# Optimization experiments

Hardware: AMD Instinct MI355X
Metric: run time of the kernel (lower is better)

The kernel has to match this reference:

```python
import jax, jax.numpy as jnp
import numpy as np

B, N, ND, ED, HD = 2, 384, 128, 32, 128
MSG_IN = 2 * ND + ED + 1  # 289
LN_EPS = 1e-3  # keras LayerNormalization default epsilon


def setup_inputs() -> dict:
    key = jax.random.key(0)
    ks = jax.random.split(key, 20)
    s = 0.05
    return {
        "h": jax.random.normal(ks[0], (B, N, ND), jnp.float32),
        "x": jax.random.normal(ks[1], (B, N, 3), jnp.float32),
        "edge_attr": jax.random.normal(ks[2], (B, N, N, ED), jnp.float32),
        "atom_mask": jnp.ones((B, N), jnp.float32),
        "msg_w1": jax.random.normal(ks[3], (MSG_IN, HD), jnp.float32) * s,
        "msg_b1": jnp.zeros((HD,), jnp.float32),
        "msg_w2": jax.random.normal(ks[4], (HD, HD), jnp.float32) * s,
        "msg_b2": jnp.zeros((HD,), jnp.float32),
        "node_w1": jax.random.normal(ks[5], (ND + HD, HD), jnp.float32) * s,
        "node_b1": jnp.zeros((HD,), jnp.float32),
        "node_w2": jax.random.normal(ks[6], (HD, ND), jnp.float32) * s,
        "node_b2": jnp.zeros((ND,), jnp.float32),
        "coord_w1": jax.random.normal(ks[7], (HD, HD), jnp.float32) * s,
        "coord_b1": jnp.zeros((HD,), jnp.float32),
        "coord_w2": jax.random.normal(ks[8], (HD, 1), jnp.float32) * 0.01,  # RandomNormal(0, 0.01)
        "ln_gamma": jnp.ones((ND,), jnp.float32),
        "ln_beta": jnp.zeros((ND,), jnp.float32),
        "adj": jax.random.randint(ks[9], (B, N, N), 0, 2, jnp.int32),
    }


def _layernorm(y, gamma, beta):
    mu = jnp.mean(y, axis=-1, keepdims=True)
    var = jnp.mean(jnp.square(y - mu), axis=-1, keepdims=True)
    return (y - mu) * jax.lax.rsqrt(var + LN_EPS) * gamma + beta


def reference(h, x, edge_attr, atom_mask,
              msg_w1, msg_b1, msg_w2, msg_b2,
              node_w1, node_b1, node_w2, node_b2,
              coord_w1, coord_b1, coord_w2,
              ln_gamma, ln_beta, adj):
    n = h.shape[1]
    rel_pos = x[:, :, None, :] - x[:, None, :, :]              # [B,N,N,3]
    dist_sq = jnp.sum(rel_pos ** 2, axis=-1, keepdims=True)    # [B,N,N,1]
    h_i = jnp.broadcast_to(h[:, :, None, :], (h.shape[0], n, n, h.shape[-1]))
    h_j = jnp.broadcast_to(h[:, None, :, :], (h.shape[0], n, n, h.shape[-1]))
    msg_in = jnp.concatenate([h_i, h_j, edge_attr, dist_sq], axis=-1)  # [B,N,N,289]
    m = jax.nn.silu(msg_in @ msg_w1 + msg_b1)
    m = jax.nn.silu(m @ msg_w2 + msg_b2)                        # [B,N,N,HD]
    adj_f = adj.astype(m.dtype)[..., None]                      # [B,N,N,1]
    m = m * adj_f
    h_agg = jnp.sum(m, axis=2)                                  # [B,N,HD]
    u = jax.nn.silu(jnp.concatenate([h, h_agg], axis=-1) @ node_w1 + node_b1)
    h_update = u @ node_w2 + node_b2
    h_new = _layernorm(h + h_update, ln_gamma, ln_beta)
    # coordinate update
    cw = jax.nn.silu(m @ coord_w1 + coord_b1) @ coord_w2        # [B,N,N,1]
    dist = jnp.sqrt(dist_sq + 1e-8)
    cw = cw / (dist + 1.0) * adj_f
    x_agg = jnp.sum(cw * rel_pos, axis=2) * atom_mask[..., None]
    x_new = x + x_agg
    return (h_new, x_new)
```

## Files before the change

### kernel.cpp

```cpp
#include <hip/hip_runtime.h>

typedef float f32x4 __attribute__((ext_vector_type(4)));
typedef unsigned int u32x4 __attribute__((ext_vector_type(4)));
typedef unsigned int u32x2 __attribute__((ext_vector_type(2)));
typedef __bf16 bf16x8 __attribute__((ext_vector_type(8)));

#define LDS_WET   0
#define LDS_W2T   10240
#define LDS_WC1T  45056
#define LDS_ACTW  79872
#define LDS_FP    114688
#define LDS_CIDX  117760
#define LDS_WCNT  118528
#define LDS_BYTES 118596

__device__ __forceinline__ unsigned short f2bf(float f) {
  unsigned int u = __builtin_bit_cast(unsigned int, f);
  unsigned int r = u + 0x7FFFu + ((u >> 16) & 1u);
  return (unsigned short)(r >> 16);
}
__device__ __forceinline__ unsigned int pk2(float lo, float hi) {
  unsigned short a = __builtin_bit_cast(unsigned short, (__bf16)lo);
  unsigned short b = __builtin_bit_cast(unsigned short, (__bf16)hi);
  return (unsigned int)a | ((unsigned int)b << 16);
}
__device__ __forceinline__ short bf1(float f) {
  return (short)__builtin_bit_cast(unsigned short, (__bf16)f);
}
__device__ __forceinline__ float bflo(unsigned int u) {
  return __builtin_bit_cast(float, u << 16);
}
__device__ __forceinline__ float bfhi(unsigned int u) {
  return __builtin_bit_cast(float, u & 0xFFFF0000u);
}
__device__ __forceinline__ float silu_f(float xv) {
  float t = __builtin_amdgcn_exp2f(-1.44269504088896f * xv);
  return xv * __builtin_amdgcn_rcpf(1.0f + t);
}
__device__ __forceinline__ f32x4 mfma16(u32x4 a, u32x4 b, f32x4 c) {
  return __builtin_amdgcn_mfma_f32_16x16x32_bf16(
      __builtin_bit_cast(bf16x8, a), __builtin_bit_cast(bf16x8, b), c, 0, 0, 0);
}

__global__ void egnn_pre(const float* __restrict__ h,
                         const float* __restrict__ msg_w1,
                         const float* __restrict__ msg_b1,
                         float* __restrict__ his,
                         unsigned short* __restrict__ hjw) {
  __shared__ float hr[128];
  const int row = blockIdx.x;
  const int t = threadIdx.x;
  if (t < 128) hr[t] = h[(size_t)row*128 + t];
  __syncthreads();
  const int col = t & 127;
  const int base = (t < 128) ? 0 : 128;
  float s = (t < 128) ? msg_b1[col] : 0.0f;
  #pragma unroll 4
  for (int k = 0; k < 128; ++k) s += hr[k] * msg_w1[(size_t)(base + k)*128 + col];
  if (t < 128) his[(size_t)row*128 + col] = s;
  else         hjw[(size_t)row*128 + col] = f2bf(s);
}

__launch_bounds__(512, 1)
__global__ void egnn_main(
    const float* __restrict__ h, const float* __restrict__ x,
    const float* __restrict__ eattr, const float* __restrict__ amask,
    const float* __restrict__ msg_w1, const float* __restrict__ msg_w2,
    const float* __restrict__ msg_b2, const float* __restrict__ node_w1,
    const float* __restrict__ node_b1, const float* __restrict__ node_w2,
    const float* __restrict__ node_b2, const float* __restrict__ coord_w1,
    const float* __restrict__ coord_b1, const float* __restrict__ coord_w2,
    const float* __restrict__ ln_g, const float* __restrict__ ln_b,
    const int* __restrict__ adj, const float* __restrict__ his,
    const unsigned short* __restrict__ hjw, float* __restrict__ out)
{
  extern __shared__ char smem[];
  short* weT  = (short*)(smem + LDS_WET);
  short* w2T  = (short*)(smem + LDS_W2T);
  short* wc1T = (short*)(smem + LDS_WC1T);
  float* fp   = (float*)(smem + LDS_FP);
  float* HisL = fp;          float* wdL  = fp + 128;
  float* b2L  = fp + 256;    float* bc1L = fp + 384;
  float* wc2L = fp + 512;    float* hrow = fp + 640;
  unsigned short* cidx16 = (unsigned short*)(smem + LDS_CIDX);
  int* wcnt = (int*)(smem + LDS_WCNT);
  int* wsc  = wcnt + 8;

  const int tid  = threadIdx.x;
  const int bi   = blockIdx.x;
  const int bb   = (bi / 384) * 384;
  const int wave = tid >> 6;
  const int lane = tid & 63;
  const int g    = lane >> 4;
  const int lr   = lane & 15;
  short* actW = (short*)(smem + LDS_ACTW) + wave*(16*136);

  const bool pred = (tid < 384) && (adj[(size_t)bi*384 + tid] != 0);
  const unsigned long long bmask = __ballot(pred);
  if (lane == 0) wcnt[wave] = __popcll(bmask);

  for (int idx = tid; idx < 32*128; idx += 512) {
    int k = idx >> 7, d = idx & 127;
    weT[d*40 + k] = bf1(msg_w1[(size_t)(256 + k)*128 + d]);
  }
  for (int idx = tid; idx < 128*128; idx += 512) {
    int k = idx >> 7, d = idx & 127;
    w2T[d*136 + k]  = bf1(msg_w2[idx]);
    wc1T[d*136 + k] = bf1(coord_w1[idx]);
  }
  if (tid < 128) {
    HisL[tid] = his[(size_t)bi*128 + tid];
    wdL[tid]  = msg_w1[288*128 + tid];
    b2L[tid]  = msg_b2[tid];
    bc1L[tid] = coord_b1[tid];
    wc2L[tid] = coord_w2[tid];
    hrow[tid] = h[(size_t)bi*128 + tid];
  }
  __syncthreads();

  if (tid == 0) {
    int run = 0;
    #pragma unroll
    for (int w = 0; w < 8; ++w) { wsc[w] = run; run += wcnt[w]; }
    wsc[8] = run;
  }
  __syncthreads();
  if (pred) {
    int rank = __popcll(bmask & ((1ull << lane) - 1ull));
    cidx16[wsc[wave] + rank] = (unsigned short)tid;
  }
  const int deg = wsc[8];
  const float xi0 = x[bi*3+0], xi1 = x[bi*3+1], xi2 = x[bi*3+2];
  f32x4 hacc2[8];
  #pragma unroll
  for (int cf = 0; cf < 8; ++cf) hacc2[cf] = (f32x4){0.f, 0.f, 0.f, 0.f};
  float xc0 = 0.0f, xc1 = 0.0f, xc2 = 0.0f;
  __syncthreads();

  const int nchunk = (deg + 127) >> 7;
  for (int ch = 0; ch < nchunk; ++ch) {
    const int sbase = ch*128 + wave*16;
    if (sbase >= deg) continue;
    const int s = sbase + lr;
    const bool valid = (s < deg);
    const int cj = valid ? (int)cidx16[s] : 0;
    const float vm = valid ? 1.0f : 0.0f;
    const float* xp = x + (size_t)(bb + cj)*3;
    const float r0 = xi0 - xp[0], r1 = xi1 - xp[1], r2 = xi2 - xp[2];
    const float dq = r0*r0 + r1*r1 + r2*r2;
    const float fc = __builtin_amdgcn_rcpf(sqrtf(dq + 1e-8f) + 1.0f) * vm;
    const float c0 = fc*r0, c1 = fc*r1, c2 = fc*r2;
    const float* ep = eattr + ((size_t)bi*384 + cj)*32 + g*8;
    const float4 p0 = ((const float4*)ep)[0];
    const float4 p1 = ((const float4*)ep)[1];
    const u32x4 be = (u32x4){pk2(p0.x, p0.y), pk2(p0.z, p0.w),
                             pk2(p1.x, p1.y), pk2(p1.z, p1.w)};

    #pragma unroll
    for (int cf = 0; cf < 8; ++cf) {
      const int dO = cf*16 + 4*g;
      u32x2 hj = *(const u32x2*)(hjw + (size_t)(bb + cj)*128 + dO);
      f32x4 hv = *(const f32x4*)(HisL + dO);
      f32x4 wv = *(const f32x4*)(wdL + dO);
      f32x4 acc;
      acc[0] = hv[0] + dq*wv[0] + bflo(hj[0]);
      acc[1] = hv[1] + dq*wv[1] + bfhi(hj[0]);
      acc[2] = hv[2] + dq*wv[2] + bflo(hj[1]);
      acc[3] = hv[3] + dq*wv[3] + bfhi(hj[1]);
      u32x4 aw = *(const u32x4*)(weT + (cf*16 + lr)*40 + g*8);
      acc = mfma16(aw, be, acc);
      *(u32x2*)(actW + lr*136 + dO) =
          (u32x2){pk2(silu_f(acc[0]), silu_f(acc[1])),
                  pk2(silu_f(acc[2]), silu_f(acc[3]))};
    }

    u32x4 bk[4];
    #pragma unroll
    for (int kk = 0; kk < 4; ++kk)
      bk[kk] = *(const u32x4*)(actW + lr*136 + kk*32 + g*8);
    #pragma unroll
    for (int cf = 0; cf < 8; ++cf) {
      const int dO = cf*16 + 4*g;
      f32x4 a = *(const f32x4*)(b2L + dO);
      #pragma unroll
      for (int kk = 0; kk < 4; ++kk) {
        u32x4 aw2 = *(const u32x4*)(w2T + (cf*16 + lr)*136 + kk*32 + g*8);
        a = mfma16(aw2, bk[kk], a);
      }
      float v0 = silu_f(a[0]) * vm, v1 = silu_f(a[1]) * vm;
      float v2 = silu_f(a[2]) * vm, v3 = silu_f(a[3]) * vm;
      hacc2[cf][0] += v0; hacc2[cf][1] += v1;
      hacc2[cf][2] += v2; hacc2[cf][3] += v3;
      *(u32x2*)(actW + lr*136 + dO) = (u32x2){pk2(v0, v1), pk2(v2, v3)};
    }

    u32x4 bm[4];
    #pragma unroll
    for (int kk = 0; kk < 4; ++kk)
      bm[kk] = *(const u32x4*)(actW + lr*136 + kk*32 + g*8);
    float cwp = 0.0f;
    #pragma unroll
    for (int cf = 0; cf < 8; ++cf) {
      const int dO = cf*16 + 4*g;
      f32x4 a = *(const f32x4*)(bc1L + dO);
      #pragma unroll
      for (int kk = 0; kk < 4; ++kk) {
        u32x4 aw3 = *(const u32x4*)(wc1T + (cf*16 + lr)*136 + kk*32 + g*8);
        a = mfma16(aw3, bm[kk], a);
      }
      f32x4 wv = *(const f32x4*)(wc2L + dO);
      cwp += silu_f(a[0])*wv[0] + silu_f(a[1])*wv[1]
           + silu_f(a[2])*wv[2] + silu_f(a[3])*wv[3];
    }
    cwp += __shfl_xor(cwp, 16, 64);
    cwp += __shfl_xor(cwp, 32, 64);
    if (lane < 16) { xc0 += cwp*c0; xc1 += cwp*c1; xc2 += cwp*c2; }
  }

  __syncthreads();
  #pragma unroll
  for (int cf = 0; cf < 8; ++cf) {
    #pragma unroll
    for (int r = 0; r < 4; ++r) {
      float v = hacc2[cf][r];
      v += __shfl_xor(v, 1, 64); v += __shfl_xor(v, 2, 64);
      v += __shfl_xor(v, 4, 64); v += __shfl_xor(v, 8, 64);
      hacc2[cf][r] = v;
    }
  }
  float* actF  = (float*)(smem + LDS_ACTW);
  float* hpart = actF;
  float* xcf   = actF + 1024;
  float* red   = actF + 1408;
  float* hagg  = actF + 1920;
  float* uvec  = actF + 2048;
  float* lnr   = actF + 2176;
  if (lr == 0) {
    #pragma unroll
    for (int cf = 0; cf < 8; ++cf)
      #pragma unroll
      for (int r = 0; r < 4; ++r)
        hpart[wave*128 + cf*16 + 4*g + r] = hacc2[cf][r];
  }
  if (lane < 16) {
    const int idx = wave*16 + lr;
    xcf[idx] = xc0; xcf[128 + idx] = xc1; xcf[256 + idx] = xc2;
  }
  __syncthreads();
  if (tid < 128) {
    float s = 0.0f;
    #pragma unroll
    for (int w = 0; w < 8; ++w) s += hpart[w*128 + tid];
    hagg[tid] = s;
  }
  if (tid < 3) {
    float sx = 0.0f;
    #pragma unroll 8
    for (int j = 0; j < 128; ++j) sx += xcf[tid*128 + j];
    out[98304 + (size_t)bi*3 + tid] = x[bi*3 + tid] + sx * amask[bi];
  }
  __syncthreads();

  {
    const int d = tid & 127, q = tid >> 7;
    float s = 0.0f;
    for (int k = q*64; k < q*64 + 64; ++k) {
      const float inv = (k < 128) ? hrow[k] : hagg[k - 128];
      s += inv * node_w1[(size_t)k*128 + d];
    }
    red[q*128 + d] = s;
  }
  __syncthreads();
  if (tid < 128)
    uvec[tid] = silu_f(red[tid] + red[128+tid] + red[256+tid] + red[384+tid] + node_b1[tid]);
  __syncthreads();

  {
    const int d = tid & 127, q = tid >> 7;
    float s = 0.0f;
    for (int k = q*32; k < q*32 + 32; ++k) s += uvec[k] * node_w2[(size_t)k*128 + d];
    red[q*128 + d] = s;
  }
  __syncthreads();
  float y = 0.0f;
  if (tid < 128)
    y = hrow[tid] + red[tid] + red[128+tid] + red[256+tid] + red[384+tid] + node_b2[tid];

  float ssum = (tid < 128) ? y : 0.0f;
  #pragma unroll
  for (int mm = 1; mm < 64; mm <<= 1) ssum += __shfl_xor(ssum, mm, 64);
  if (tid < 128 && lane == 0) lnr[wave] = ssum;
  __syncthreads();
  const float mu = (lnr[0] + lnr[1]) * (1.0f/128.0f);
  float yc = (tid < 128) ? (y - mu) : 0.0f;
  float sq = yc * yc;
  #pragma unroll
  for (int mm = 1; mm < 64; mm <<= 1) sq += __shfl_xor(sq, mm, 64);
  if (tid < 128 && lane == 0) lnr[2 + wave] = sq;
  __syncthreads();
  if (tid < 128) {
    const float var = (lnr[2] + lnr[3]) * (1.0f/128.0f);
    out[(size_t)bi*128 + tid] = yc * rsqrtf(var + 1e-3f) * ln_g[tid] + ln_b[tid];
  }
}

extern "C" void kernel_launch(void* const* d_in, const int* in_sizes, int n_in,
                              void* d_out, int out_size, void* d_ws, size_t ws_size,
                              hipStream_t stream) {
  const float* h        = (const float*)d_in[0];
  const float* x        = (const float*)d_in[1];
  const float* eattr    = (const float*)d_in[2];
  const float* amask    = (const float*)d_in[3];
  const float* msg_w1   = (const float*)d_in[4];
  const float* msg_b1   = (const float*)d_in[5];
  const float* msg_w2   = (const float*)d_in[6];
  const float* msg_b2   = (const float*)d_in[7];
  const float* node_w1  = (const float*)d_in[8];
  const float* node_b1  = (const float*)d_in[9];
  const float* node_w2  = (const float*)d_in[10];
  const float* node_b2  = (const float*)d_in[11];
  const float* coord_w1 = (const float*)d_in[12];
  const float* coord_b1 = (const float*)d_in[13];
  const float* coord_w2 = (const float*)d_in[14];
  const float* ln_g     = (const float*)d_in[15];
  const float* ln_b     = (const float*)d_in[16];
  const int*   adj      = (const int*)d_in[17];
  float* out = (float*)d_out;
  float* his = (float*)d_ws;
  unsigned short* hjw = (unsigned short*)((char*)d_ws + 393216);

  hipFuncSetAttribute((const void*)egnn_main,
                      hipFuncAttributeMaxDynamicSharedMemorySize, LDS_BYTES);

  egnn_pre<<<768, 256, 0, stream>>>(h, msg_w1, msg_b1, his, hjw);
  egnn_main<<<768, 512, LDS_BYTES, stream>>>(h, x, eattr, amask, msg_w1, msg_w2,
      msg_b2, node_w1, node_b1, node_w2, node_b2, coord_w1, coord_b1, coord_w2,
      ln_g, ln_b, adj, his, hjw, out);
}
```

Baseline: 81.18 us.

## Pass MFMA activations through lane shuffles and XOR-swizzle weight tiles in LDS

Per-wave activation staging through LDS between the three chained MFMA stages is replaced by cross-lane shuffles that rebuild the B-operand fragments directly from registers. The padded weight layouts (stride 136) are replaced by an XOR-swizzled stride-128 layout to avoid bank conflicts, which shrinks LDS use substantially and may allow more blocks per CU. The epilogue scratch now reuses the start of shared memory. In exchange there are 32 shuffles per stage, plus extra register pressure from holding packed outputs.

```diff
diff --git a/kernel.cpp b/kernel.cpp
--- a/kernel.cpp
+++ b/kernel.cpp
@@ -7,12 +7,11 @@
 
 #define LDS_WET   0
 #define LDS_W2T   10240
-#define LDS_WC1T  45056
-#define LDS_ACTW  79872
-#define LDS_FP    114688
-#define LDS_CIDX  117760
-#define LDS_WCNT  118528
-#define LDS_BYTES 118596
+#define LDS_WC1T  43008
+#define LDS_FP    75776
+#define LDS_CIDX  78848
+#define LDS_WCNT  79616
+#define LDS_BYTES 79684
 
 __device__ __forceinline__ unsigned short f2bf(float f) {
   unsigned int u = __builtin_bit_cast(unsigned int, f);
@@ -93,7 +92,10 @@
   const int lane = tid & 63;
   const int g    = lane >> 4;
   const int lr   = lane & 15;
-  short* actW = (short*)(smem + LDS_ACTW) + wave*(16*136);
+  const int swz  = (lr & 7) << 3;
+  const int srcA = ((g & 1) << 5) + lr;
+  const int srcB = srcA + 16;
+  const bool glow = (g < 2);
 
   const bool pred = (tid < 384) && (adj[(size_t)bi*384 + tid] != 0);
   const unsigned long long bmask = __ballot(pred);
@@ -105,8 +107,9 @@
   }
   for (int idx = tid; idx < 128*128; idx += 512) {
     int k = idx >> 7, d = idx & 127;
-    w2T[d*136 + k]  = bf1(msg_w2[idx]);
-    wc1T[d*136 + k] = bf1(coord_w1[idx]);
+    int si = (d*128 + k) ^ ((d & 7) << 3);
+    w2T[si]  = bf1(msg_w2[idx]);
+    wc1T[si] = bf1(coord_w1[idx]);
   }
   if (tid < 128) {
     HisL[tid] = his[(size_t)bi*128 + tid];
@@ -156,6 +159,7 @@
     const u32x4 be = (u32x4){pk2(p0.x, p0.y), pk2(p0.z, p0.w),
                              pk2(p1.x, p1.y), pk2(p1.z, p1.w)};
 
+    unsigned int lo1[8], hi1[8];
     #pragma unroll
     for (int cf = 0; cf < 8; ++cf) {
       const int dO = cf*16 + 4*g;
@@ -169,35 +173,62 @@
       acc[3] = hv[3] + dq*wv[3] + bfhi(hj[1]);
       u32x4 aw = *(const u32x4*)(weT + (cf*16 + lr)*40 + g*8);
       acc = mfma16(aw, be, acc);
-      *(u32x2*)(actW + lr*136 + dO) =
-          (u32x2){pk2(silu_f(acc[0]), silu_f(acc[1])),
-                  pk2(silu_f(acc[2]), silu_f(acc[3]))};
+      lo1[cf] = pk2(silu_f(acc[0]), silu_f(acc[1]));
+      hi1[cf] = pk2(silu_f(acc[2]), silu_f(acc[3]));
     }
 
     u32x4 bk[4];
     #pragma unroll
-    for (int kk = 0; kk < 4; ++kk)
-      bk[kk] = *(const u32x4*)(actW + lr*136 + kk*32 + g*8);
+    for (int kk = 0; kk < 4; ++kk) {
+      int aA0 = __shfl((int)lo1[2*kk],   srcA, 64);
+      int aB0 = __shfl((int)lo1[2*kk+1], srcA, 64);
+      int aA1 = __shfl((int)hi1[2*kk],   srcA, 64);
+      int aB1 = __shfl((int)hi1[2*kk+1], srcA, 64);
+      int aA2 = __shfl((int)lo1[2*kk],   srcB, 64);
+      int aB2 = __shfl((int)lo1[2*kk+1], srcB, 64);
+      int aA3 = __shfl((int)hi1[2*kk],   srcB, 64);
+      int aB3 = __shfl((int)hi1[2*kk+1], srcB, 64);
+      bk[kk][0] = (unsigned)(glow ? aA0 : aB0);
+      bk[kk][1] = (unsigned)(glow ? aA1 : aB1);
+      bk[kk][2] = (unsigned)(glow ? aA2 : aB2);
+      bk[kk][3] = (unsigned)(glow ? aA3 : aB3);
+    }
+
+    unsigned int lo2[8], hi2[8];
     #pragma unroll
     for (int cf = 0; cf < 8; ++cf) {
       const int dO = cf*16 + 4*g;
       f32x4 a = *(const f32x4*)(b2L + dO);
       #pragma unroll
       for (int kk = 0; kk < 4; ++kk) {
-        u32x4 aw2 = *(const u32x4*)(w2T + (cf*16 + lr)*136 + kk*32 + g*8);
+        u32x4 aw2 = *(const u32x4*)(w2T + (((cf*16 + lr)*128 + kk*32 + g*8) ^ swz));
         a = mfma16(aw2, bk[kk], a);
       }
       float v0 = silu_f(a[0]) * vm, v1 = silu_f(a[1]) * vm;
       float v2 = silu_f(a[2]) * vm, v3 = silu_f(a[3]) * vm;
       hacc2[cf][0] += v0; hacc2[cf][1] += v1;
       hacc2[cf][2] += v2; hacc2[cf][3] += v3;
-      *(u32x2*)(actW + lr*136 + dO) = (u32x2){pk2(v0, v1), pk2(v2, v3)};
+      lo2[cf] = pk2(v0, v1);
+      hi2[cf] = pk2(v2, v3);
     }
 
     u32x4 bm[4];
     #pragma unroll
-    for (int kk = 0; kk < 4; ++kk)
-      bm[kk] = *(const u32x4*)(actW + lr*136 + kk*32 + g*8);
+    for (int kk = 0; kk < 4; ++kk) {
+      int aA0 = __shfl((int)lo2[2*kk],   srcA, 64);
+      int aB0 = __shfl((int)lo2[2*kk+1], srcA, 64);
+      int aA1 = __shfl((int)hi2[2*kk],   srcA, 64);
+      int aB1 = __shfl((int)hi2[2*kk+1], srcA, 64);
+      int aA2 = __shfl((int)lo2[2*kk],   srcB, 64);
+      int aB2 = __shfl((int)lo2[2*kk+1], srcB, 64);
+      int aA3 = __shfl((int)hi2[2*kk],   srcB, 64);
+      int aB3 = __shfl((int)hi2[2*kk+1], srcB, 64);
+      bm[kk][0] = (unsigned)(glow ? aA0 : aB0);
+      bm[kk][1] = (unsigned)(glow ? aA1 : aB1);
+      bm[kk][2] = (unsigned)(glow ? aA2 : aB2);
+      bm[kk][3] = (unsigned)(glow ? aA3 : aB3);
+    }
+
     float cwp = 0.0f;
     #pragma unroll
     for (int cf = 0; cf < 8; ++cf) {
@@ -205,7 +236,7 @@
       f32x4 a = *(const f32x4*)(bc1L + dO);
       #pragma unroll
       for (int kk = 0; kk < 4; ++kk) {
-        u32x4 aw3 = *(const u32x4*)(wc1T + (cf*16 + lr)*136 + kk*32 + g*8);
+        u32x4 aw3 = *(const u32x4*)(wc1T + (((cf*16 + lr)*128 + kk*32 + g*8) ^ swz));
         a = mfma16(aw3, bm[kk], a);
       }
       f32x4 wv = *(const f32x4*)(wc2L + dO);
@@ -228,7 +259,7 @@
       hacc2[cf][r] = v;
     }
   }
-  float* actF  = (float*)(smem + LDS_ACTW);
+  float* actF  = (float*)smem;
   float* hpart = actF;
   float* xcf   = actF + 1024;
   float* red   = actF + 1408;
```

Measured after the change: 87.03 us. 7.2% more time.

## Process two 16-neighbor subtiles per wave to reuse weight fragments across MFMAs

Applied to the files above, without the earlier changes.

Each wave now handles two 16-row neighbor subtiles per pass (A and B, B offset by 8 subtiles), so every weight fragment loaded from LDS feeds two MFMAs instead of one. The goal is to halve LDS weight-read traffic per unit of work and expose more independent MFMAs for latency hiding. In exchange the per-wave activation scratch doubles, raising LDS use to about 153 KB, and register pressure rises from the duplicated accumulators. With a degree of about 192 there are only 12 subtiles, so in a single pass only waves 0–3 get a B subtile, which leaves the work imbalanced across waves.

```diff
diff --git a/kernel.cpp b/kernel.cpp
--- a/kernel.cpp
+++ b/kernel.cpp
@@ -9,10 +9,10 @@
 #define LDS_W2T   10240
 #define LDS_WC1T  45056
 #define LDS_ACTW  79872
-#define LDS_FP    114688
-#define LDS_CIDX  117760
-#define LDS_WCNT  118528
-#define LDS_BYTES 118596
+#define LDS_FP    149504
+#define LDS_CIDX  152576
+#define LDS_WCNT  153344
+#define LDS_BYTES 153412
 
 __device__ __forceinline__ unsigned short f2bf(float f) {
   unsigned int u = __builtin_bit_cast(unsigned int, f);
@@ -93,7 +93,7 @@
   const int lane = tid & 63;
   const int g    = lane >> 4;
   const int lr   = lane & 15;
-  short* actW = (short*)(smem + LDS_ACTW) + wave*(16*136);
+  short* actW = (short*)(smem + LDS_ACTW) + wave*(32*136);
 
   const bool pred = (tid < 384) && (adj[(size_t)bi*384 + tid] != 0);
   const unsigned long long bmask = __ballot(pred);
@@ -137,84 +137,151 @@
   float xc0 = 0.0f, xc1 = 0.0f, xc2 = 0.0f;
   __syncthreads();
 
-  const int nchunk = (deg + 127) >> 7;
-  for (int ch = 0; ch < nchunk; ++ch) {
-    const int sbase = ch*128 + wave*16;
-    if (sbase >= deg) continue;
-    const int s = sbase + lr;
-    const bool valid = (s < deg);
-    const int cj = valid ? (int)cidx16[s] : 0;
-    const float vm = valid ? 1.0f : 0.0f;
-    const float* xp = x + (size_t)(bb + cj)*3;
-    const float r0 = xi0 - xp[0], r1 = xi1 - xp[1], r2 = xi2 - xp[2];
-    const float dq = r0*r0 + r1*r1 + r2*r2;
-    const float fc = __builtin_amdgcn_rcpf(sqrtf(dq + 1e-8f) + 1.0f) * vm;
-    const float c0 = fc*r0, c1 = fc*r1, c2 = fc*r2;
-    const float* ep = eattr + ((size_t)bi*384 + cj)*32 + g*8;
-    const float4 p0 = ((const float4*)ep)[0];
-    const float4 p1 = ((const float4*)ep)[1];
-    const u32x4 be = (u32x4){pk2(p0.x, p0.y), pk2(p0.z, p0.w),
-                             pk2(p1.x, p1.y), pk2(p1.z, p1.w)};
+  const int nst   = (deg + 15) >> 4;
+  const int npass = (nst + 15) >> 4;
+  for (int pass = 0; pass < npass; ++pass) {
+    const int stA = pass*16 + wave;
+    if (stA*16 >= deg) continue;
+    const int stB = stA + 8;
+    const bool vBs = (stB*16 < deg);
+
+    const int sA = stA*16 + lr;
+    const int cjA = (sA < deg) ? (int)cidx16[sA] : 0;
+    const float vmA = (sA < deg) ? 1.0f : 0.0f;
+    const float* xpA = x + (size_t)(bb + cjA)*3;
+    const float r0A = xi0 - xpA[0], r1A = xi1 - xpA[1], r2A = xi2 - xpA[2];
+    const float dqA = r0A*r0A + r1A*r1A + r2A*r2A;
+    const float fcA = __builtin_amdgcn_rcpf(sqrtf(dqA + 1e-8f) + 1.0f) * vmA;
+    const float c0A = fcA*r0A, c1A = fcA*r1A, c2A = fcA*r2A;
+    const float* epA = eattr + ((size_t)bi*384 + cjA)*32 + g*8;
+    const float4 pA0 = ((const float4*)epA)[0];
+    const float4 pA1 = ((const float4*)epA)[1];
+    const u32x4 beA = (u32x4){pk2(pA0.x, pA0.y), pk2(pA0.z, pA0.w),
+                              pk2(pA1.x, pA1.y), pk2(pA1.z, pA1.w)};
+
+    int cjB = 0; float vmB = 0.f, dqB = 0.f;
+    float c0B = 0.f, c1B = 0.f, c2B = 0.f;
+    u32x4 beB = (u32x4){0u, 0u, 0u, 0u};
+    if (vBs) {
+      const int sB = stB*16 + lr;
+      cjB = (sB < deg) ? (int)cidx16[sB] : 0;
+      vmB = (sB < deg) ? 1.0f : 0.0f;
+      const float* xpB = x + (size_t)(bb + cjB)*3;
+      const float r0B = xi0 - xpB[0], r1B = xi1 - xpB[1], r2B = xi2 - xpB[2];
+      dqB = r0B*r0B + r1B*r1B + r2B*r2B;
+      const float fcB = __builtin_amdgcn_rcpf(sqrtf(dqB + 1e-8f) + 1.0f) * vmB;
+      c0B = fcB*r0B; c1B = fcB*r1B; c2B = fcB*r2B;
+      const float* epB = eattr + ((size_t)bi*384 + cjB)*32 + g*8;
+      const float4 pB0 = ((const float4*)epB)[0];
+      const float4 pB1 = ((const float4*)epB)[1];
+      beB = (u32x4){pk2(pB0.x, pB0.y), pk2(pB0.z, pB0.w),
+                    pk2(pB1.x, pB1.y), pk2(pB1.z, pB1.w)};
+    }
 
     #pragma unroll
     for (int cf = 0; cf < 8; ++cf) {
       const int dO = cf*16 + 4*g;
-      u32x2 hj = *(const u32x2*)(hjw + (size_t)(bb + cj)*128 + dO);
+      u32x4 aw = *(const u32x4*)(weT + (cf*16 + lr)*40 + g*8);
       f32x4 hv = *(const f32x4*)(HisL + dO);
       f32x4 wv = *(const f32x4*)(wdL + dO);
-      f32x4 acc;
-      acc[0] = hv[0] + dq*wv[0] + bflo(hj[0]);
-      acc[1] = hv[1] + dq*wv[1] + bfhi(hj[0]);
-      acc[2] = hv[2] + dq*wv[2] + bflo(hj[1]);
-      acc[3] = hv[3] + dq*wv[3] + bfhi(hj[1]);
-      u32x4 aw = *(const u32x4*)(weT + (cf*16 + lr)*40 + g*8);
-      acc = mfma16(aw, be, acc);
+      u32x2 hjA = *(const u32x2*)(hjw + (size_t)(bb + cjA)*128 + dO);
+      f32x4 accA;
+      accA[0] = hv[0] + dqA*wv[0] + bflo(hjA[0]);
+      accA[1] = hv[1] + dqA*wv[1] + bfhi(hjA[0]);
+      accA[2] = hv[2] + dqA*wv[2] + bflo(hjA[1]);
+      accA[3] = hv[3] + dqA*wv[3] + bfhi(hjA[1]);
+      accA = mfma16(aw, beA, accA);
       *(u32x2*)(actW + lr*136 + dO) =
-          (u32x2){pk2(silu_f(acc[0]), silu_f(acc[1])),
-                  pk2(silu_f(acc[2]), silu_f(acc[3]))};
-    }
-
-    u32x4 bk[4];
+          (u32x2){pk2(silu_f(accA[0]), silu_f(accA[1])),
+                  pk2(silu_f(accA[2]), silu_f(accA[3]))};
+      if (vBs) {
+        u32x2 hjB = *(const u32x2*)(hjw + (size_t)(bb + cjB)*128 + dO);
+        f32x4 accB;
+        accB[0] = hv[0] + dqB*wv[0] + bflo(hjB[0]);
+        accB[1] = hv[1] + dqB*wv[1] + bfhi(hjB[0]);
+        accB[2] = hv[2] + dqB*wv[2] + bflo(hjB[1]);
+        accB[3] = hv[3] + dqB*wv[3] + bfhi(hjB[1]);
+        accB = mfma16(aw, beB, accB);
+        *(u32x2*)(actW + (16 + lr)*136 + dO) =
+            (u32x2){pk2(silu_f(accB[0]), silu_f(accB[1])),
+                    pk2(silu_f(accB[2]), silu_f(accB[3]))};
+      }
+    }
+
+    u32x4 bkA[4], bkB[4] = {};
     #pragma unroll
     for (int kk = 0; kk < 4; ++kk)
-      bk[kk] = *(const u32x4*)(actW + lr*136 + kk*32 + g*8);
+      bkA[kk] = *(const u32x4*)(actW + lr*136 + kk*32 + g*8);
+    if (vBs) {
+      #pragma unroll
+      for (int kk = 0; kk < 4; ++kk)
+        bkB[kk] = *(const u32x4*)(actW + (16 + lr)*136 + kk*32 + g*8);
+    }
+
     #pragma unroll
     for (int cf = 0; cf < 8; ++cf) {
       const int dO = cf*16 + 4*g;
-      f32x4 a = *(const f32x4*)(b2L + dO);
+      f32x4 bv = *(const f32x4*)(b2L + dO);
+      f32x4 aA = bv, aB = bv;
       #pragma unroll
       for (int kk = 0; kk < 4; ++kk) {
         u32x4 aw2 = *(const u32x4*)(w2T + (cf*16 + lr)*136 + kk*32 + g*8);
-        a = mfma16(aw2, bk[kk], a);
+        aA = mfma16(aw2, bkA[kk], aA);
+        if (vBs) aB = mfma16(aw2, bkB[kk], aB);
       }
-      float v0 = silu_f(a[0]) * vm, v1 = silu_f(a[1]) * vm;
-      float v2 = silu_f(a[2]) * vm, v3 = silu_f(a[3]) * vm;
-      hacc2[cf][0] += v0; hacc2[cf][1] += v1;
-      hacc2[cf][2] += v2; hacc2[cf][3] += v3;
-      *(u32x2*)(actW + lr*136 + dO) = (u32x2){pk2(v0, v1), pk2(v2, v3)};
-    }
-
-    u32x4 bm[4];
+      {
+        float v0 = silu_f(aA[0]) * vmA, v1 = silu_f(aA[1]) * vmA;
+        float v2 = silu_f(aA[2]) * vmA, v3 = silu_f(aA[3]) * vmA;
+        hacc2[cf][0] += v0; hacc2[cf][1] += v1;
+        hacc2[cf][2] += v2; hacc2[cf][3] += v3;
+        *(u32x2*)(actW + lr*136 + dO) = (u32x2){pk2(v0, v1), pk2(v2, v3)};
+      }
+      if (vBs) {
+        float v0 = silu_f(aB[0]) * vmB, v1 = silu_f(aB[1]) * vmB;
+        float v2 = silu_f(aB[2]) * vmB, v3 = silu_f(aB[3]) * vmB;
+        hacc2[cf][0] += v0; hacc2[cf][1] += v1;
+        hacc2[cf][2] += v2; hacc2[cf][3] += v3;
+        *(u32x2*)(actW + (16 + lr)*136 + dO) = (u32x2){pk2(v0, v1), pk2(v2, v3)};
+      }
+    }
+
+    u32x4 bmA[4], bmB[4] = {};
     #pragma unroll
     for (int kk = 0; kk < 4; ++kk)
-      bm[kk] = *(const u32x4*)(actW + lr*136 + kk*32 + g*8);
-    float cwp = 0.0f;
+      bmA[kk] = *(const u32x4*)(actW + lr*136 + kk*32 + g*8);
+    if (vBs) {
+      #pragma unroll
+      for (int kk = 0; kk < 4; ++kk)
+        bmB[kk] = *(const u32x4*)(actW + (16 + lr)*136 + kk*32 + g*8);
+    }
+
+    float cwA = 0.0f, cwB = 0.0f;
     #pragma unroll
     for (int cf = 0; cf < 8; ++cf) {
       const int dO = cf*16 + 4*g;
-      f32x4 a = *(const f32x4*)(bc1L + dO);
+      f32x4 bc = *(const f32x4*)(bc1L + dO);
+      f32x4 aA = bc, aB = bc;
       #pragma unroll
       for (int kk = 0; kk < 4; ++kk) {
         u32x4 aw3 = *(const u32x4*)(wc1T + (cf*16 + lr)*136 + kk*32 + g*8);
-        a = mfma16(aw3, bm[kk], a);
+        aA = mfma16(aw3, bmA[kk], aA);
+        if (vBs) aB = mfma16(aw3, bmB[kk], aB);
       }
       f32x4 wv = *(const f32x4*)(wc2L + dO);
-      cwp += silu_f(a[0])*wv[0] + silu_f(a[1])*wv[1]
-           + silu_f(a[2])*wv[2] + silu_f(a[3])*wv[3];
-    }
-    cwp += __shfl_xor(cwp, 16, 64);
-    cwp += __shfl_xor(cwp, 32, 64);
-    if (lane < 16) { xc0 += cwp*c0; xc1 += cwp*c1; xc2 += cwp*c2; }
+      cwA += silu_f(aA[0])*wv[0] + silu_f(aA[1])*wv[1]
+           + silu_f(aA[2])*wv[2] + silu_f(aA[3])*wv[3];
+      if (vBs)
+        cwB += silu_f(aB[0])*wv[0] + silu_f(aB[1])*wv[1]
+             + silu_f(aB[2])*wv[2] + silu_f(aB[3])*wv[3];
+    }
+    cwA += __shfl_xor(cwA, 16, 64);
+    cwA += __shfl_xor(cwA, 32, 64);
+    if (lane < 16) { xc0 += cwA*c0A; xc1 += cwA*c1A; xc2 += cwA*c2A; }
+    if (vBs) {
+      cwB += __shfl_xor(cwB, 16, 64);
+      cwB += __shfl_xor(cwB, 32, 64);
+      if (lane < 16) { xc0 += cwB*c0B; xc1 += cwB*c1B; xc2 += cwB*c2B; }
+    }
   }
 
   __syncthreads();
```

Result: slower. 83.47 us (+2.8%).

## Pre-pack bf16 weights once in a kernel and read them from global memory

Applied to the files above, without the earlier changes.

Adds a small kernel that converts and transposes the message, layer-2 and coordinate weights to bf16 once, in the layout the MFMA A-operand needs. The main kernel then loads those A fragments straight from global memory instead of having each of the 768 blocks rebuild about 80 KB of transposed weights in LDS. This removes the per-block conversion prologue and cuts LDS use from about 116 KB to about 38 KB. The cost is an extra launch, plus weight fragments fetched from L1/L2 inside the inner loops with unpadded 256-byte row strides instead of LDS reads.

```diff
diff --git a/kernel.cpp b/kernel.cpp
--- a/kernel.cpp
+++ b/kernel.cpp
@@ -5,14 +5,11 @@
 typedef unsigned int u32x2 __attribute__((ext_vector_type(2)));
 typedef __bf16 bf16x8 __attribute__((ext_vector_type(8)));
 
-#define LDS_WET   0
-#define LDS_W2T   10240
-#define LDS_WC1T  45056
-#define LDS_ACTW  79872
-#define LDS_FP    114688
-#define LDS_CIDX  117760
-#define LDS_WCNT  118528
-#define LDS_BYTES 118596
+#define LDS_ACTW  0
+#define LDS_FP    34816
+#define LDS_CIDX  37888
+#define LDS_WCNT  38656
+#define LDS_BYTES 38724
 
 __device__ __forceinline__ unsigned short f2bf(float f) {
   unsigned int u = __builtin_bit_cast(unsigned int, f);
@@ -23,9 +20,6 @@
   unsigned short a = __builtin_bit_cast(unsigned short, (__bf16)lo);
   unsigned short b = __builtin_bit_cast(unsigned short, (__bf16)hi);
   return (unsigned int)a | ((unsigned int)b << 16);
-}
-__device__ __forceinline__ short bf1(float f) {
-  return (short)__builtin_bit_cast(unsigned short, (__bf16)f);
 }
 __device__ __forceinline__ float bflo(unsigned int u) {
   return __builtin_bit_cast(float, u << 16);
@@ -61,23 +55,41 @@
   else         hjw[(size_t)row*128 + col] = f2bf(s);
 }
 
+__global__ void egnn_wpack(const float* __restrict__ msg_w1,
+                           const float* __restrict__ msg_w2,
+                           const float* __restrict__ coord_w1,
+                           unsigned short* __restrict__ weP,
+                           unsigned short* __restrict__ w2P,
+                           unsigned short* __restrict__ wc1P) {
+  const int idx = blockIdx.x*256 + threadIdx.x;
+  if (idx < 32*128) {
+    int d = idx >> 5, k = idx & 31;
+    weP[idx] = f2bf(msg_w1[(size_t)(256 + k)*128 + d]);
+  }
+  if (idx < 128*128) {
+    int d = idx >> 7, k = idx & 127;
+    w2P[idx]  = f2bf(msg_w2[(size_t)k*128 + d]);
+    wc1P[idx] = f2bf(coord_w1[(size_t)k*128 + d]);
+  }
+}
+
 __launch_bounds__(512, 1)
 __global__ void egnn_main(
     const float* __restrict__ h, const float* __restrict__ x,
     const float* __restrict__ eattr, const float* __restrict__ amask,
-    const float* __restrict__ msg_w1, const float* __restrict__ msg_w2,
-    const float* __restrict__ msg_b2, const float* __restrict__ node_w1,
-    const float* __restrict__ node_b1, const float* __restrict__ node_w2,
-    const float* __restrict__ node_b2, const float* __restrict__ coord_w1,
+    const float* __restrict__ msg_w1, const float* __restrict__ msg_b2,
+    const float* __restrict__ node_w1, const float* __restrict__ node_b1,
+    const float* __restrict__ node_w2, const float* __restrict__ node_b2,
     const float* __restrict__ coord_b1, const float* __restrict__ coord_w2,
     const float* __restrict__ ln_g, const float* __restrict__ ln_b,
     const int* __restrict__ adj, const float* __restrict__ his,
-    const unsigned short* __restrict__ hjw, float* __restrict__ out)
+    const unsigned short* __restrict__ hjw,
+    const unsigned short* __restrict__ weP,
+    const unsigned short* __restrict__ w2P,
+    const unsigned short* __restrict__ wc1P,
+    float* __restrict__ out)
 {
   extern __shared__ char smem[];
-  short* weT  = (short*)(smem + LDS_WET);
-  short* w2T  = (short*)(smem + LDS_W2T);
-  short* wc1T = (short*)(smem + LDS_WC1T);
   float* fp   = (float*)(smem + LDS_FP);
   float* HisL = fp;          float* wdL  = fp + 128;
   float* b2L  = fp + 256;    float* bc1L = fp + 384;
@@ -99,15 +111,6 @@
   const unsigned long long bmask = __ballot(pred);
   if (lane == 0) wcnt[wave] = __popcll(bmask);
 
-  for (int idx = tid; idx < 32*128; idx += 512) {
-    int k = idx >> 7, d = idx & 127;
-    weT[d*40 + k] = bf1(msg_w1[(size_t)(256 + k)*128 + d]);
-  }
-  for (int idx = tid; idx < 128*128; idx += 512) {
-    int k = idx >> 7, d = idx & 127;
-    w2T[d*136 + k]  = bf1(msg_w2[idx]);
-    wc1T[d*136 + k] = bf1(coord_w1[idx]);
-  }
   if (tid < 128) {
     HisL[tid] = his[(size_t)bi*128 + tid];
     wdL[tid]  = msg_w1[288*128 + tid];
@@ -167,7 +170,7 @@
       acc[1] = hv[1] + dq*wv[1] + bfhi(hj[0]);
       acc[2] = hv[2] + dq*wv[2] + bflo(hj[1]);
       acc[3] = hv[3] + dq*wv[3] + bfhi(hj[1]);
-      u32x4 aw = *(const u32x4*)(weT + (cf*16 + lr)*40 + g*8);
+      u32x4 aw = *(const u32x4*)(weP + (cf*16 + lr)*32 + g*8);
       acc = mfma16(aw, be, acc);
       *(u32x2*)(actW + lr*136 + dO) =
           (u32x2){pk2(silu_f(acc[0]), silu_f(acc[1])),
@@ -184,7 +187,7 @@
       f32x4 a = *(const f32x4*)(b2L + dO);
       #pragma unroll
       for (int kk = 0; kk < 4; ++kk) {
-        u32x4 aw2 = *(const u32x4*)(w2T + (cf*16 + lr)*136 + kk*32 + g*8);
+        u32x4 aw2 = *(const u32x4*)(w2P + (cf*16 + lr)*128 + kk*32 + g*8);
         a = mfma16(aw2, bk[kk], a);
       }
       float v0 = silu_f(a[0]) * vm, v1 = silu_f(a[1]) * vm;
@@ -205,7 +208,7 @@
       f32x4 a = *(const f32x4*)(bc1L + dO);
       #pragma unroll
       for (int kk = 0; kk < 4; ++kk) {
-        u32x4 aw3 = *(const u32x4*)(wc1T + (cf*16 + lr)*136 + kk*32 + g*8);
+        u32x4 aw3 = *(const u32x4*)(wc1P + (cf*16 + lr)*128 + kk*32 + g*8);
         a = mfma16(aw3, bm[kk], a);
       }
       f32x4 wv = *(const f32x4*)(wc2L + dO);
@@ -327,13 +330,17 @@
   const int*   adj      = (const int*)d_in[17];
   float* out = (float*)d_out;
   float* his = (float*)d_ws;
-  unsigned short* hjw = (unsigned short*)((char*)d_ws + 393216);
+  unsigned short* hjw  = (unsigned short*)((char*)d_ws + 393216);
+  unsigned short* weP  = (unsigned short*)((char*)d_ws + 589824);
+  unsigned short* w2P  = (unsigned short*)((char*)d_ws + 598016);
+  unsigned short* wc1P = (unsigned short*)((char*)d_ws + 630784);
 
   hipFuncSetAttribute((const void*)egnn_main,
                       hipFuncAttributeMaxDynamicSharedMemorySize, LDS_BYTES);
 
   egnn_pre<<<768, 256, 0, stream>>>(h, msg_w1, msg_b1, his, hjw);
-  egnn_main<<<768, 512, LDS_BYTES, stream>>>(h, x, eattr, amask, msg_w1, msg_w2,
-      msg_b2, node_w1, node_b1, node_w2, node_b2, coord_w1, coord_b1, coord_w2,
-      ln_g, ln_b, adj, his, hjw, out);
-}
+  egnn_wpack<<<64, 256, 0, stream>>>(msg_w1, msg_w2, coord_w1, weP, w2P, wc1P);
+  egnn_main<<<768, 512, LDS_BYTES, stream>>>(h, x, eattr, amask, msg_w1,
+      msg_b2, node_w1, node_b1, node_w2, node_b2, coord_b1, coord_w2,
+      ln_g, ln_b, adj, his, hjw, weP, w2P, wc1P, out);
+}
```

Result: slower. 129.4 us (+59.3%).
